# Performance work log

Hardware: AMD Instinct MI355X
Metric: run time of the kernel (lower is better)

Reference implementation:

```python
import jax, jax.numpy as jnp
import numpy as np

BS, S, N, C, H, CP, T, CT, NB = 1, 2, 2048, 128, 8, 16, 512, 384, 3
DH = C // H
INF = 1.0e8

def _ln(x, w, b, eps=1e-5):
    mu = jnp.mean(x, axis=-1, keepdims=True)
    var = jnp.var(x, axis=-1, keepdims=True)
    return (x - mu) * jax.lax.rsqrt(var + eps) * w + b

def _ln_na(x, eps=1e-5):
    mu = jnp.mean(x, axis=-1, keepdims=True)
    var = jnp.var(x, axis=-1, keepdims=True)
    return (x - mu) * jax.lax.rsqrt(var + eps)

def _betas(n):
    # query row l belongs to window centered at 32*(l//32)+16; keys within +/- n_keys//2=64
    l = jnp.arange(n)
    centers = (l // 32) * 32 + 16
    m = jnp.arange(n)
    ok = (m[None, :] >= (centers - 64)[:, None]) & (m[None, :] < (centers + 64)[:, None])
    return jnp.where(ok, 0.0, -INF).astype(jnp.float32)

def setup_inputs():
    key = jax.random.key(0)
    ks = iter(jax.random.split(key, 80))
    def W(*shape):
        return jax.random.normal(next(ks), shape, dtype=jnp.float32) * 0.05
    return {
        "atom_single": jax.random.normal(next(ks), (BS, S, N, C), dtype=jnp.float32),
        "atom_proj": jax.random.normal(next(ks), (BS, N, C), dtype=jnp.float32),
        "atom_pair": jax.random.normal(next(ks), (BS, N, N, CP), dtype=jnp.float32),
        "mask": jnp.ones((BS, N), jnp.float32),
        "tok_idx": jnp.sort(jax.random.randint(next(ks), (BS, N), 0, T), axis=-1),
        "aln_s_w": jnp.ones((NB, C), jnp.float32), "aln_s_b": jnp.zeros((NB, C), jnp.float32),
        "aln_gate_w": W(NB, C, C), "aln_gate_b": jnp.zeros((NB, C), jnp.float32),
        "aln_shift_w": W(NB, C, C),
        "q_w": W(NB, C, C), "q_b": jnp.zeros((NB, C), jnp.float32),
        "k_w": W(NB, C, C), "v_w": W(NB, C, C),
        "pair_ln_w": jnp.ones((NB, CP), jnp.float32), "pair_ln_b": jnp.zeros((NB, CP), jnp.float32),
        "pair_w": W(NB, CP, H),
        "gate_w": W(NB, C, C), "out_w": W(NB, C, C),
        "og_w": W(NB, C, C), "og_b": jnp.full((NB, C), -2.0, jnp.float32),
        "t_aln_s_w": jnp.ones((NB, C), jnp.float32), "t_aln_s_b": jnp.zeros((NB, C), jnp.float32),
        "t_aln_gate_w": W(NB, C, C), "t_aln_gate_b": jnp.zeros((NB, C), jnp.float32),
        "t_aln_shift_w": W(NB, C, C),
        "t_a_w": W(NB, C, 2 * C), "t_b_w": W(NB, C, 2 * C),
        "t_out_w": W(NB, 2 * C, C),
        "t_og_w": W(NB, C, C), "t_og_b": jnp.full((NB, C), -2.0, jnp.float32),
        "tok_w": W(C, CT),
    }

def _forward(atom_single, atom_proj, atom_pair, mask, tok_idx, aln_s_w, aln_s_b, aln_gate_w, aln_gate_b, aln_shift_w, q_w, q_b, k_w, v_w, pair_ln_w, pair_ln_b, pair_w, gate_w, out_w, og_w, og_b, t_aln_s_w, t_aln_s_b, t_aln_gate_w, t_aln_gate_b, t_aln_shift_w, t_a_w, t_b_w, t_out_w, t_og_w, t_og_b, tok_w):
    betas = _betas(N)[None, None, None]                        # [1,1,1,N,N]
    mask_bias = ((mask - 1.0) * INF)[:, None, None, None, :]   # [bs,1,1,1,N]
    s = atom_proj[:, None]                                     # [bs,1,N,C]
    a = atom_single                                            # [bs,S,N,C]
    for i in range(NB):
        # AttentionPairBias with AdaLN conditioning on s
        sn = _ln(s, aln_s_w[i], aln_s_b[i])
        a1 = jax.nn.sigmoid(sn @ aln_gate_w[i] + aln_gate_b[i]) * _ln_na(a) + sn @ aln_shift_w[i]
        q = (a1 @ q_w[i] + q_b[i]).reshape(BS, S, N, H, DH)
        k = (a1 @ k_w[i]).reshape(BS, S, N, H, DH)
        v = (a1 @ v_w[i]).reshape(BS, S, N, H, DH)
        zb = _ln(atom_pair, pair_ln_w[i], pair_ln_b[i]) @ pair_w[i]    # [bs,N,N,H]
        zb = jnp.transpose(zb, (0, 3, 1, 2))[:, None]                  # [bs,1,H,N,N]
        logits = jnp.einsum('bsqhd,bskhd->bshqk', q, k) / np.float32(np.sqrt(DH)) + zb + betas + mask_bias
        p = jax.nn.softmax(logits, axis=-1)
        o = jnp.einsum('bshqk,bskhd->bsqhd', p, v).reshape(BS, S, N, C)
        o = (jax.nn.sigmoid(a1 @ gate_w[i]) * o) @ out_w[i]
        a = a + jax.nn.sigmoid(sn @ og_w[i] + og_b[i]) * o
        # ConditionedTransitionBlock (SwiGLU with adaLN-Zero gating)
        sn2 = _ln(s, t_aln_s_w[i], t_aln_s_b[i])
        a2 = jax.nn.sigmoid(sn2 @ t_aln_gate_w[i] + t_aln_gate_b[i]) * _ln_na(a) + sn2 @ t_aln_shift_w[i]
        hidden = jax.nn.silu(a2 @ t_a_w[i]) * (a2 @ t_b_w[i])
        a = a + jax.nn.sigmoid(sn2 @ t_og_w[i] + t_og_b[i]) * (hidden @ t_out_w[i])
    # project to token dim, relu, scatter-mean atoms -> tokens
    q_tok = jax.nn.relu(a @ tok_w)                             # [bs,S,N,CT]
    oh = jax.nn.one_hot(tok_idx, T, dtype=q_tok.dtype)         # [bs,N,T]
    cnt = jnp.clip(jnp.sum(oh, axis=1), 1.0)                   # [bs,T]
    tok = jnp.einsum('bsnc,bnt->bstc', q_tok, oh) / cnt[:, None, :, None]
    return tok

def reference(atom_single, atom_proj, atom_pair, mask, tok_idx, aln_s_w, aln_s_b, aln_gate_w, aln_gate_b, aln_shift_w, q_w, q_b, k_w, v_w, pair_ln_w, pair_ln_b, pair_w, gate_w, out_w, og_w, og_b, t_aln_s_w, t_aln_s_b, t_aln_gate_w, t_aln_gate_b, t_aln_shift_w, t_a_w, t_b_w, t_out_w, t_og_w, t_og_b, tok_w):
    return _forward(atom_single, atom_proj, atom_pair, mask, tok_idx, aln_s_w, aln_s_b, aln_gate_w, aln_gate_b, aln_shift_w, q_w, q_b, k_w, v_w, pair_ln_w, pair_ln_b, pair_w, gate_w, out_w, og_w, og_b, t_aln_s_w, t_aln_s_b, t_aln_gate_w, t_aln_gate_b, t_aln_shift_w, t_a_w, t_b_w, t_out_w, t_og_w, t_og_b, tok_w)
```

## Files before the change

### kernel.cpp

```cpp
#include <hip/hip_runtime.h>
#include <math.h>

#define NATOM 2048
#define CD 128
#define SD 2
#define TT 512
#define CTD 384
#define NBI 3
#define MR 4096

typedef unsigned short ushortx;
typedef __attribute__((ext_vector_type(8))) short bf16x8;
typedef __attribute__((ext_vector_type(4))) float f32x4;
typedef __attribute__((ext_vector_type(4))) unsigned short us4;

__device__ __forceinline__ float sigm(float x){ return 1.0f/(1.0f+expf(-x)); }
__device__ __forceinline__ ushortx f2b(float f){
  union { float f; unsigned u; } v; v.f = f;
  unsigned r = v.u + 0x7fffu + ((v.u>>16)&1u);
  return (ushortx)(r>>16);
}
__device__ __forceinline__ float b2f(ushortx u){
  union { unsigned u; float f; } v; v.u = ((unsigned)u)<<16; return v.f;
}
union U8 { ushortx u[8]; float4 v; };

__device__ __forceinline__ void unpack8(float* dst, float4 v){
  U8 pk; pk.v = v;
  #pragma unroll
  for (int t=0;t<8;t++) dst[t] = b2f(pk.u[t]);
}

#define OFFB_W3T    0ll
#define OFFB_B3     589824ll
#define OFFB_WQKVGT 599040ll
#define OFFB_BQ     992256ll
#define OFFB_WOUTT  998400ll
#define OFFB_WABT   1096704ll
#define OFFB_WTOUTT 1489920ll
#define OFFB_WTOKT  1686528ll
#define OFFB_A1     1784832ll
#define OFFB_SNP    2833408ll
#define OFFB_A      12270592ll
#define OFFB_QKVG   14367744ll
#define OFFB_ZB     18562048ll
#define OFFB_QTOK   31144960ll

struct WPtrs {
  const float *aln_gate_w, *aln_gate_b, *aln_shift_w, *og_w, *og_b;
  const float *t_aln_gate_w, *t_aln_gate_b, *t_aln_shift_w, *t_og_w, *t_og_b;
  const float *q_w, *q_b, *k_w, *v_w, *gate_w, *out_w;
  const float *t_a_w, *t_b_w, *t_out_w, *tok_w;
};

__global__ __launch_bounds__(256) void prologue_kernel(WPtrs P, char* __restrict__ wsb,
  const float* __restrict__ atom_single, const float* __restrict__ atom_pair,
  const float* __restrict__ plw, const float* __restrict__ plb, const float* __restrict__ pw)
{
  int b = blockIdx.x;
  if (b < 3471){
    long long idx = (long long)b*256 + threadIdx.x;
    const long long s0=294912, s1=2304, s2=196608, s3=1536, s4=49152, s5=196608, s6=98304;
    if (idx < s0) {
      int which = (int)(idx/49152); int r = (int)(idx%49152); int n=r/128, k=r%128;
      int i = which>>1, t = which&1;
      const float* src;
      if (n<128)      src = (t?P.t_aln_gate_w :P.aln_gate_w ) + i*16384 + k*128 + n;
      else if (n<256) src = (t?P.t_aln_shift_w:P.aln_shift_w) + i*16384 + k*128 + (n-128);
      else            src = (t?P.t_og_w       :P.og_w       ) + i*16384 + k*128 + (n-256);
      ((ushortx*)(wsb+OFFB_W3T))[idx] = f2b(*src); return;
    }
    idx -= s0;
    if (idx < s1) {
      int which = (int)(idx/384); int col = (int)(idx%384); int i=which>>1, t=which&1;
      float v = 0.f;
      if (col<128)       v = (t?P.t_aln_gate_b:P.aln_gate_b)[i*128+col];
      else if (col>=256) v = (t?P.t_og_b      :P.og_b      )[i*128+col-256];
      ((float*)(wsb+OFFB_B3))[idx] = v; return;
    }
    idx -= s1;
    if (idx < s2) {
      int i = (int)(idx/65536); int r = (int)(idx%65536); int n=r/128, k=r%128;
      int seg = n>>7, c = n&127;
      const float* src = (seg==0?P.q_w: seg==1?P.k_w: seg==2?P.v_w: P.gate_w) + i*16384 + k*128 + c;
      ((ushortx*)(wsb+OFFB_WQKVGT))[idx] = f2b(*src); return;
    }
    idx -= s2;
    if (idx < s3) {
      int i = (int)(idx/512); int col = (int)(idx%512);
      ((float*)(wsb+OFFB_BQ))[idx] = (col<128) ? P.q_b[i*128+col] : 0.f; return;
    }
    idx -= s3;
    if (idx < s4) {
      int i = (int)(idx/16384); int r = (int)(idx%16384); int n=r/128, k=r%128;
      ((ushortx*)(wsb+OFFB_WOUTT))[idx] = f2b(P.out_w[i*16384 + k*128 + n]); return;
    }
    idx -= s4;
    if (idx < s5) {
      int i = (int)(idx/65536); int r = (int)(idx%65536); int n=r/128, k=r%128;
      const float* src = (n<256) ? P.t_a_w + i*32768 + k*256 + n
                                 : P.t_b_w + i*32768 + k*256 + (n-256);
      ((ushortx*)(wsb+OFFB_WABT))[idx] = f2b(*src); return;
    }
    idx -= s5;
    if (idx < s6) {
      int i = (int)(idx/32768); int r = (int)(idx%32768); int n=r/256, k=r%256;
      ((ushortx*)(wsb+OFFB_WTOUTT))[idx] = f2b(P.t_out_w[i*32768 + k*128 + n]); return;
    }
    idx -= s6;
    {
      int n = (int)(idx/128); int k = (int)(idx%128);
      ((ushortx*)(wsb+OFFB_WTOKT))[idx] = f2b(P.tok_w[k*384 + n]); return;
    }
  }
  if (b < 5519){
    int i = (b-3471)*256 + threadIdx.x;
    ((float*)(wsb+OFFB_A))[i] = atom_single[i];
    return;
  }
  {
    int idx = (b-5519)*256 + threadIdx.x;
    int q = idx>>7, j = idx&127;
    int m = (q & ~31) - 48 + j;
    bool ok = (m>=0 && m<NATOM);
    float x[16]; float mu=0.f, rs=0.f;
    if (ok){
      float s=0.f, sq=0.f;
      const float* p = atom_pair + ((long long)q*NATOM + m)*16;
      #pragma unroll
      for (int c=0;c<16;c++){ x[c]=p[c]; s+=x[c]; sq+=x[c]*x[c]; }
      mu = s*(1.f/16.f); float var = sq*(1.f/16.f)-mu*mu; rs = rsqrtf(var+1e-5f);
    }
    ushortx* zb = (ushortx*)(wsb+OFFB_ZB);
    #pragma unroll
    for (int it=0; it<NBI; it++){
      float out[8] = {0,0,0,0,0,0,0,0};
      if (ok){
        #pragma unroll
        for (int c=0;c<16;c++){
          float xn = (x[c]-mu)*rs*plw[it*16+c] + plb[it*16+c];
          #pragma unroll
          for (int h=0;h<8;h++) out[h] += xn * pw[it*128 + c*8 + h];
        }
      }
      #pragma unroll
      for (int h=0;h<8;h++)
        zb[(((long long)it*8+h)*NATOM + q)*128 + j] = f2b(out[h]);
    }
  }
}

__global__ __launch_bounds__(256) void attn_kernel(const ushortx* __restrict__ qkvg,
  const ushortx* __restrict__ zb, const float* __restrict__ mask, ushortx* __restrict__ og)
{
  int qb = blockIdx.x, h = blockIdx.y, s = blockIdx.z;
  int base = qb*32 - 48;
  __shared__ float Qs[32][20], Ks[128][20], Vs[128][20], Ls[32][132], maskb[128];
  __shared__ float redx[32][8], rowv[32];
  int tid = threadIdx.x;
  for (int idx=tid; idx<32*2; idx+=256){
    int r=idx>>1, d8=(idx&1)*8;
    float4 v = *(const float4*)&qkvg[((long long)(s*NATOM + qb*32 + r))*512 + h*16 + d8];
    unpack8(&Qs[r][d8], v);
  }
  for (int idx=tid; idx<512; idx+=256){
    int j = idx&127, d8 = ((idx>>7)&1)*8, kv = idx>>8;
    int m = base + j; int mc = m<0?0:(m>NATOM-1?NATOM-1:m);
    long long row = ((long long)(s*NATOM + mc))*512;
    float4 v = *(const float4*)&qkvg[row + (kv?256:128) + h*16 + d8];
    if (kv) unpack8(&Vs[j][d8], v); else unpack8(&Ks[j][d8], v);
  }
  if (tid < 128){
    int m = base + tid;
    maskb[tid] = (m>=0 && m<NATOM) ? (mask[m]-1.0f)*1e8f : -1e30f;
  }
  __syncthreads();
  int r = tid>>3, g = tid&7;
  {
    float4 q0=*(float4*)&Qs[r][0], q1=*(float4*)&Qs[r][4], q2=*(float4*)&Qs[r][8], q3=*(float4*)&Qs[r][12];
    const ushortx* zrow = zb + ((long long)h*NATOM + (qb*32+r))*128;
    #pragma unroll
    for (int j=g; j<128; j+=8){
      float4 k0=*(float4*)&Ks[j][0], k1=*(float4*)&Ks[j][4], k2=*(float4*)&Ks[j][8], k3=*(float4*)&Ks[j][12];
      float dot = q0.x*k0.x + q0.y*k0.y + q0.z*k0.z + q0.w*k0.w
                + q1.x*k1.x + q1.y*k1.y + q1.z*k1.z + q1.w*k1.w
                + q2.x*k2.x + q2.y*k2.y + q2.z*k2.z + q2.w*k2.w
                + q3.x*k3.x + q3.y*k3.y + q3.z*k3.z + q3.w*k3.w;
      Ls[r][j] = dot*0.25f + b2f(zrow[j]) + maskb[j];
    }
  }
  __syncthreads();
  float pmax = -1e30f;
  for (int j=g*16; j<g*16+16; j++) pmax = fmaxf(pmax, Ls[r][j]);
  redx[r][g] = pmax; __syncthreads();
  if (g==0){ float mx=redx[r][0]; for(int u=1;u<8;u++) mx=fmaxf(mx,redx[r][u]); rowv[r]=mx; }
  __syncthreads();
  float mx = rowv[r];
  float psum = 0.f;
  for (int j=g*16; j<g*16+16; j++){ float e = expf(Ls[r][j]-mx); Ls[r][j]=e; psum += e; }
  redx[r][g] = psum; __syncthreads();
  if (g==0){ float sm=0.f; for(int u=0;u<8;u++) sm+=redx[r][u]; rowv[r]=sm; }
  __syncthreads();
  {
    int q2=tid>>3, dg=(tid>>1)&3, jh=tid&1;
    float4 acc = make_float4(0.f,0.f,0.f,0.f);
    for (int j=jh*64; j<jh*64+64; j++){
      float p = Ls[q2][j];
      float4 v = *(float4*)&Vs[j][dg*4];
      acc.x += p*v.x; acc.y += p*v.y; acc.z += p*v.z; acc.w += p*v.w;
    }
    acc.x += __shfl_xor(acc.x,1); acc.y += __shfl_xor(acc.y,1);
    acc.z += __shfl_xor(acc.z,1); acc.w += __shfl_xor(acc.w,1);
    if (jh==0){
      long long mrow = (long long)(s*NATOM + qb*32 + q2);
      float inv = 1.0f / rowv[q2];
      us4 gt = *(const us4*)&qkvg[mrow*512 + 384 + h*16 + dg*4];
      us4 st;
      st[0] = f2b(sigm(b2f(gt[0]))*acc.x*inv);
      st[1] = f2b(sigm(b2f(gt[1]))*acc.y*inv);
      st[2] = f2b(sigm(b2f(gt[2]))*acc.z*inv);
      st[3] = f2b(sigm(b2f(gt[3]))*acc.w*inv);
      *(us4*)(og + mrow*128 + h*16 + dg*4) = st;
    }
  }
}

template<int AM, int BM>
__global__ __launch_bounds__(256) void gemm_f(
    const void* __restrict__ Asrc, long long strideA,
    const ushortx* __restrict__ B, long long strideB,
    const float* __restrict__ bias, long long strideBias,
    void* Cv, long long strideC,
    int M, int N, int K, int mode,
    const ushortx* __restrict__ gate, int gate_ld, int gate_coloff,
    const void* __restrict__ p1, const void* __restrict__ p2,
    const void* __restrict__ p3, const void* __restrict__ p4)
{
  constexpr int CG  = 256/BM;
  constexpr int XC  = 128/CG;
  constexpr int F4  = XC/8;
  constexpr int ACI = BM/32;
  int z = blockIdx.z;
  B += z*strideB;
  if (bias) bias += z*strideBias;
  float* C = (float*)Cv + z*strideC;
  ushortx* Cu = (ushortx*)Cv + z*strideC;
  __shared__ ushortx At[BM][136];
  __shared__ ushortx Bt[64][136];
  int tid = threadIdx.x;
  int rowBase = blockIdx.y*BM, colBase = blockIdx.x*64;
  int wave = tid>>6, lane = tid&63;
  int wr = (wave>>1)*(BM/2), wc = (wave&1)*32;
  int lr = lane&15, lk = (lane>>4)*8;
  f32x4 acc[ACI][2];
  #pragma unroll
  for (int i=0;i<ACI;i++)
    #pragma unroll
    for (int j=0;j<2;j++) acc[i][j] = (f32x4){0.f,0.f,0.f,0.f};

  int sr = tid/CG, q = tid%CG, cs = q*XC;
  int row = rowBase + sr;
  int bsr = tid>>2, bq = tid&3, bcs = bq*32;

  for (int kc=0; kc<K; kc+=128){
    if (kc) __syncthreads();
    if (AM==0){
      const ushortx* Ab = (const ushortx*)Asrc + z*strideA;
      const float4* ag = (const float4*)(Ab + (long long)row*K + kc + cs);
      #pragma unroll
      for (int u=0;u<F4;u++) *(float4*)&At[sr][cs+u*8] = ag[u];
    } else if (AM==3){
      const float* Af_ = (const float*)Asrc;
      const float4* ar = (const float4*)(Af_ + (long long)row*128 + cs);
      #pragma unroll
      for (int u=0;u<F4;u++){
        float4 a = ar[2*u], b = ar[2*u+1];
        U8 pk;
        pk.u[0]=f2b(a.x); pk.u[1]=f2b(a.y); pk.u[2]=f2b(a.z); pk.u[3]=f2b(a.w);
        pk.u[4]=f2b(b.x); pk.u[5]=f2b(b.y); pk.u[6]=f2b(b.z); pk.u[7]=f2b(b.w);
        *(float4*)&At[sr][cs+u*8] = pk.v;
      }
    } else if (AM==2){
      const ushortx* hp = (const ushortx*)Asrc;
      const float4* xr = (const float4*)(hp + (long long)row*512 + kc + cs);
      const float4* yr = (const float4*)(hp + (long long)row*512 + 256 + kc + cs);
      #pragma unroll
      for (int u=0;u<F4;u++){
        U8 xa, ya, pk;
        xa.v = xr[u]; ya.v = yr[u];
        #pragma unroll
        for (int t=0;t<8;t++){
          float x = b2f(xa.u[t]), y = b2f(ya.u[t]);
          pk.u[t] = f2b(x*sigm(x)*y);
        }
        *(float4*)&At[sr][cs+u*8] = pk.v;
      }
    } else {
      const float* arow = (const float*)Asrc + (long long)row*128;
      float x[XC]; float s=0.f, sq=0.f;
      const float4* ar = (const float4*)(arow + cs);
      #pragma unroll
      for (int u=0;u<XC/4;u++){
        float4 t = ar[u];
        x[4*u]=t.x; x[4*u+1]=t.y; x[4*u+2]=t.z; x[4*u+3]=t.w;
        s += t.x+t.y+t.z+t.w;
        sq += t.x*t.x+t.y*t.y+t.z*t.z+t.w*t.w;
      }
      #pragma unroll
      for (int off=1; off<CG; off<<=1){ s += __shfl_xor(s,off); sq += __shfl_xor(sq,off); }
      float mu = s*(1.f/128.f), var = sq*(1.f/128.f)-mu*mu;
      float rs = rsqrtf(var + 1e-5f);
      if (AM==1){
        const ushortx* sp = (const ushortx*)p1 + (long long)(row & (NATOM-1))*384;
        const float4* gr = (const float4*)(sp + cs);
        const float4* hr = (const float4*)(sp + 128 + cs);
        #pragma unroll
        for (int u=0;u<F4;u++){
          U8 ga, ha, pk;
          ga.v = gr[u]; ha.v = hr[u];
          #pragma unroll
          for (int t=0;t<8;t++)
            pk.u[t] = f2b(sigm(b2f(ga.u[t]))*((x[8*u+t]-mu)*rs) + b2f(ha.u[t]));
          *(float4*)&At[sr][cs+u*8] = pk.v;
        }
      } else {
        int iw = z>>1, tw = z&1;
        const float* w = (const float*)(tw?p3:p1) + iw*128;
        const float* b = (const float*)(tw?p4:p2) + iw*128;
        const float4* wrp = (const float4*)(w + cs);
        const float4* brp = (const float4*)(b + cs);
        #pragma unroll
        for (int u=0;u<F4;u++){
          float4 wa = wrp[2*u], wb = wrp[2*u+1];
          float4 ba = brp[2*u], bb = brp[2*u+1];
          U8 pk;
          pk.u[0]=f2b((x[8*u  ]-mu)*rs*wa.x+ba.x);
          pk.u[1]=f2b((x[8*u+1]-mu)*rs*wa.y+ba.y);
          pk.u[2]=f2b((x[8*u+2]-mu)*rs*wa.z+ba.z);
          pk.u[3]=f2b((x[8*u+3]-mu)*rs*wa.w+ba.w);
          pk.u[4]=f2b((x[8*u+4]-mu)*rs*wb.x+bb.x);
          pk.u[5]=f2b((x[8*u+5]-mu)*rs*wb.y+bb.y);
          pk.u[6]=f2b((x[8*u+6]-mu)*rs*wb.z+bb.z);
          pk.u[7]=f2b((x[8*u+7]-mu)*rs*wb.w+bb.w);
          *(float4*)&At[sr][cs+u*8] = pk.v;
        }
      }
    }
    {
      const float4* bg = (const float4*)(B + (long long)(colBase+bsr)*K + kc + bcs);
      #pragma unroll
      for (int u=0;u<4;u++) *(float4*)&Bt[bsr][bcs+u*8] = bg[u];
    }
    __syncthreads();
    #pragma unroll
    for (int ks=0; ks<4; ks++){
      bf16x8 b0 = *(const bf16x8*)&Bt[wc+lr][ks*32+lk];
      bf16x8 b1 = *(const bf16x8*)&Bt[wc+16+lr][ks*32+lk];
      #pragma unroll
      for (int i=0;i<ACI;i++){
        bf16x8 a = *(const bf16x8*)&At[wr+i*16+lr][ks*32+lk];
        acc[i][0] = __builtin_amdgcn_mfma_f32_16x16x32_bf16(a,b0,acc[i][0],0,0,0);
        acc[i][1] = __builtin_amdgcn_mfma_f32_16x16x32_bf16(a,b1,acc[i][1],0,0,0);
      }
    }
  }
  int crow0 = rowBase + wr + (lane>>4)*4;
  int ccol0 = colBase + wc + lr;
  #pragma unroll
  for (int i=0;i<ACI;i++){
    #pragma unroll
    for (int j=0;j<2;j++){
      int col = ccol0 + j*16;
      float bv = bias ? bias[col] : 0.f;
      #pragma unroll
      for (int rr=0; rr<4; rr++){
        int rrow = crow0 + i*16 + rr;
        float v = acc[i][j][rr] + bv;
        long long ci = (long long)rrow*N + col;
        if (mode==1) C[ci] = fmaxf(v, 0.f);
        else if (mode==2){
          int n = rrow & (NATOM-1);
          C[ci] += sigm(b2f(gate[(long long)n*gate_ld + gate_coloff + col])) * v;
        } else if (mode==3) Cu[ci] = f2b(v);
        else if (mode==4) Cu[ci] = f2b(fmaxf(v, 0.f));
        else C[ci] = v;
      }
    }
  }
}

__global__ __launch_bounds__(128) void tokagg_kernel(const int* __restrict__ tok_idx,
    const float* __restrict__ qtok, float* __restrict__ out)
{
  int t = blockIdx.x;
  int lo=0, hi=NATOM;
  while (lo<hi){ int mid=(lo+hi)>>1; if (tok_idx[mid] < t) lo=mid+1; else hi=mid; }
  int start = lo;
  lo = start; hi = NATOM;
  while (lo<hi){ int mid=(lo+hi)>>1; if (tok_idx[mid] <= t) lo=mid+1; else hi=mid; }
  int end = lo;
  int cnt = end - start;
  float inv = 1.0f / (float)(cnt>0 ? cnt : 1);
  for (int s=0; s<SD; s++)
    for (int c=threadIdx.x; c<CTD; c+=128){
      float acc = 0.f;
      for (int n=start; n<end; n++) acc += qtok[((long long)(s*NATOM+n))*CTD + c];
      out[(long long)(s*TT + t)*CTD + c] = acc*inv;
    }
}

extern "C" void kernel_launch(void* const* d_in, const int* in_sizes, int n_in,
                              void* d_out, int out_size, void* d_ws, size_t ws_size,
                              hipStream_t stream)
{
  const float* atom_single = (const float*)d_in[0];
  const float* atom_proj   = (const float*)d_in[1];
  const float* atom_pair   = (const float*)d_in[2];
  const float* mask        = (const float*)d_in[3];
  const int*   tok_idx     = (const int*)  d_in[4];
  const float* aln_s_w     = (const float*)d_in[5];
  const float* aln_s_b     = (const float*)d_in[6];
  const float* pair_ln_w   = (const float*)d_in[14];
  const float* pair_ln_b   = (const float*)d_in[15];
  const float* pair_w      = (const float*)d_in[16];
  const float* t_aln_s_w   = (const float*)d_in[21];
  const float* t_aln_s_b   = (const float*)d_in[22];

  char* wsb = (char*)d_ws;
  ushortx* W3T    = (ushortx*)(wsb+OFFB_W3T);
  float*   B3     = (float*)  (wsb+OFFB_B3);
  ushortx* WQKVGT = (ushortx*)(wsb+OFFB_WQKVGT);
  float*   BQ     = (float*)  (wsb+OFFB_BQ);
  ushortx* WOUTT  = (ushortx*)(wsb+OFFB_WOUTT);
  ushortx* WABT   = (ushortx*)(wsb+OFFB_WABT);
  ushortx* WTOUTT = (ushortx*)(wsb+OFFB_WTOUTT);
  ushortx* WTOKT  = (ushortx*)(wsb+OFFB_WTOKT);
  ushortx* A1     = (ushortx*)(wsb+OFFB_A1);
  ushortx* SNP    = (ushortx*)(wsb+OFFB_SNP);
  float*   Af     = (float*)  (wsb+OFFB_A);
  ushortx* QKVG   = (ushortx*)(wsb+OFFB_QKVG);
  ushortx* ZB     = (ushortx*)(wsb+OFFB_ZB);
  float*   QTOK   = (float*)  (wsb+OFFB_QTOK);

  WPtrs P;
  P.aln_gate_w=(const float*)d_in[7];  P.aln_gate_b=(const float*)d_in[8];  P.aln_shift_w=(const float*)d_in[9];
  P.og_w=(const float*)d_in[19]; P.og_b=(const float*)d_in[20];
  P.t_aln_gate_w=(const float*)d_in[23]; P.t_aln_gate_b=(const float*)d_in[24]; P.t_aln_shift_w=(const float*)d_in[25];
  P.t_og_w=(const float*)d_in[29]; P.t_og_b=(const float*)d_in[30];
  P.q_w=(const float*)d_in[10]; P.q_b=(const float*)d_in[11]; P.k_w=(const float*)d_in[12];
  P.v_w=(const float*)d_in[13]; P.gate_w=(const float*)d_in[17]; P.out_w=(const float*)d_in[18];
  P.t_a_w=(const float*)d_in[26]; P.t_b_w=(const float*)d_in[27]; P.t_out_w=(const float*)d_in[28];
  P.tok_w=(const float*)d_in[31];

  prologue_kernel<<<6543,256,0,stream>>>(P, wsb, atom_single, atom_pair,
      pair_ln_w, pair_ln_b, pair_w);
  gemm_f<4,64><<<dim3(6,32,6),256,0,stream>>>(atom_proj, 0, W3T, 49152ll,
      B3, 384ll, SNP, 786432ll, NATOM, 384, 128, 3, nullptr, 0, 0,
      aln_s_w, aln_s_b, t_aln_s_w, t_aln_s_b);

  for (int i=0;i<NBI;i++){
    const ushortx* snpA = SNP + (long long)(2*i)*786432;
    const ushortx* snpT = SNP + (long long)(2*i+1)*786432;
    gemm_f<1,64><<<dim3(8,64,1),256,0,stream>>>(Af, 0, WQKVGT + (long long)i*65536, 0,
        BQ + (long long)i*512, 0, QKVG, 0, MR, 512, 128, 3, nullptr, 0, 0,
        snpA, nullptr, nullptr, nullptr);
    attn_kernel<<<dim3(64,8,2),256,0,stream>>>(QKVG, ZB + (long long)i*2097152, mask, A1);
    gemm_f<0,32><<<dim3(2,128,1),256,0,stream>>>(A1, 0, WOUTT + (long long)i*16384, 0,
        nullptr, 0, Af, 0, MR, 128, 128, 2, snpA, 384, 256,
        nullptr, nullptr, nullptr, nullptr);
    gemm_f<1,64><<<dim3(8,64,1),256,0,stream>>>(Af, 0, WABT + (long long)i*65536, 0,
        nullptr, 0, QKVG, 0, MR, 512, 128, 3, nullptr, 0, 0,
        snpT, nullptr, nullptr, nullptr);
    gemm_f<2,32><<<dim3(2,128,1),256,0,stream>>>(QKVG, 0, WTOUTT + (long long)i*32768, 0,
        nullptr, 0, Af, 0, MR, 128, 256, 2, snpT, 384, 256,
        nullptr, nullptr, nullptr, nullptr);
  }
  gemm_f<3,64><<<dim3(6,64,1),256,0,stream>>>(Af, 0, WTOKT, 0, nullptr, 0,
      QTOK, 0, MR, CTD, 128, 1, nullptr, 0, 0,
      nullptr, nullptr, nullptr, nullptr);
  tokagg_kernel<<<TT,128,0,stream>>>(tok_idx, QTOK, (float*)d_out);
}
```

Baseline: 601.0 us.

## Fuse post-attention GEMM chain and next QKVG projection into one kernel

```diff
diff --git a/kernel.cpp b/kernel.cpp
--- a/kernel.cpp
+++ b/kernel.cpp
@@ -155,8 +155,11 @@
 {
   int qb = blockIdx.x, h = blockIdx.y, s = blockIdx.z;
   int base = qb*32 - 48;
-  __shared__ float Qs[32][20], Ks[128][20], Vs[128][20], Ls[32][132], maskb[128];
-  __shared__ float redx[32][8], rowv[32];
+  __shared__ __align__(16) float Qs[32][20];
+  __shared__ __align__(16) ushortx KsU[128][24];
+  __shared__ __align__(16) ushortx VsU[128][24];
+  __shared__ __align__(16) float Ls[32][132];
+  __shared__ float maskb[128], redx[32][8], rowv[32];
   int tid = threadIdx.x;
   for (int idx=tid; idx<32*2; idx+=256){
     int r=idx>>1, d8=(idx&1)*8;
@@ -168,7 +171,7 @@
     int m = base + j; int mc = m<0?0:(m>NATOM-1?NATOM-1:m);
     long long row = ((long long)(s*NATOM + mc))*512;
     float4 v = *(const float4*)&qkvg[row + (kv?256:128) + h*16 + d8];
-    if (kv) unpack8(&Vs[j][d8], v); else unpack8(&Ks[j][d8], v);
+    if (kv) *(float4*)&VsU[j][d8] = v; else *(float4*)&KsU[j][d8] = v;
   }
   if (tid < 128){
     int m = base + tid;
@@ -181,11 +184,11 @@
     const ushortx* zrow = zb + ((long long)h*NATOM + (qb*32+r))*128;
     #pragma unroll
     for (int j=g; j<128; j+=8){
-      float4 k0=*(float4*)&Ks[j][0], k1=*(float4*)&Ks[j][4], k2=*(float4*)&Ks[j][8], k3=*(float4*)&Ks[j][12];
-      float dot = q0.x*k0.x + q0.y*k0.y + q0.z*k0.z + q0.w*k0.w
-                + q1.x*k1.x + q1.y*k1.y + q1.z*k1.z + q1.w*k1.w
-                + q2.x*k2.x + q2.y*k2.y + q2.z*k2.z + q2.w*k2.w
-                + q3.x*k3.x + q3.y*k3.y + q3.z*k3.z + q3.w*k3.w;
+      U8 ka, kb; ka.v = *(const float4*)&KsU[j][0]; kb.v = *(const float4*)&KsU[j][8];
+      float dot = q0.x*b2f(ka.u[0]) + q0.y*b2f(ka.u[1]) + q0.z*b2f(ka.u[2]) + q0.w*b2f(ka.u[3])
+                + q1.x*b2f(ka.u[4]) + q1.y*b2f(ka.u[5]) + q1.z*b2f(ka.u[6]) + q1.w*b2f(ka.u[7])
+                + q2.x*b2f(kb.u[0]) + q2.y*b2f(kb.u[1]) + q2.z*b2f(kb.u[2]) + q2.w*b2f(kb.u[3])
+                + q3.x*b2f(kb.u[4]) + q3.y*b2f(kb.u[5]) + q3.z*b2f(kb.u[6]) + q3.w*b2f(kb.u[7]);
       Ls[r][j] = dot*0.25f + b2f(zrow[j]) + maskb[j];
     }
   }
@@ -206,8 +209,9 @@
     float4 acc = make_float4(0.f,0.f,0.f,0.f);
     for (int j=jh*64; j<jh*64+64; j++){
       float p = Ls[q2][j];
-      float4 v = *(float4*)&Vs[j][dg*4];
-      acc.x += p*v.x; acc.y += p*v.y; acc.z += p*v.z; acc.w += p*v.w;
+      us4 vv = *(const us4*)&VsU[j][dg*4];
+      acc.x += p*b2f(vv[0]); acc.y += p*b2f(vv[1]);
+      acc.z += p*b2f(vv[2]); acc.w += p*b2f(vv[3]);
     }
     acc.x += __shfl_xor(acc.x,1); acc.y += __shfl_xor(acc.y,1);
     acc.z += __shfl_xor(acc.z,1); acc.w += __shfl_xor(acc.w,1);
@@ -221,6 +225,152 @@
       st[2] = f2b(sigm(b2f(gt[2]))*acc.z*inv);
       st[3] = f2b(sigm(b2f(gt[3]))*acc.w*inv);
       *(us4*)(og + mrow*128 + h*16 + dg*4) = st;
+    }
+  }
+}
+
+template<int LAST>
+__global__ __launch_bounds__(256) void postattn_kernel(
+  float* __restrict__ Af, const ushortx* __restrict__ A1,
+  const ushortx* __restrict__ Wout,
+  const ushortx* __restrict__ Wab,
+  const ushortx* __restrict__ Wtout,
+  const ushortx* __restrict__ WN,
+  const float*   __restrict__ biasN,
+  const ushortx* __restrict__ snpA,
+  const ushortx* __restrict__ snpT,
+  const ushortx* __restrict__ snpN,
+  ushortx* __restrict__ QKVG,
+  float*   __restrict__ QTOK)
+{
+  __shared__ __align__(16) ushortx Bt[2][64][136];
+  __shared__ __align__(16) float   Afr[16][132];
+  __shared__ __align__(16) ushortx A2t[16][136];
+  __shared__ __align__(16) ushortx Ht[16][264];
+  __shared__ __align__(16) ushortx XX[16*264];
+  ushortx (*A1t)[136] = (ushortx(*)[136])XX;
+  ushortx (*Hs)[264]  = (ushortx(*)[264])XX;
+
+  int tid=threadIdx.x, rowBase=blockIdx.x*16;
+  int wave=tid>>6, lane=tid&63, lr=lane&15, lk=(lane>>4)*8;
+  int wc = wave*16;
+  int r=tid>>4, c8=(tid&15)*8;
+  long long grow = rowBase + r;
+  int sr=tid>>2, csB=(tid&3)*32;
+  int crow = (lane>>4)*4;
+
+  *(float4*)&A1t[r][c8] = *(const float4*)&A1[grow*128 + c8];
+  { const float4* ap=(const float4*)&Af[grow*128+c8];
+    *(float4*)&Afr[r][c8]=ap[0]; *(float4*)&Afr[r][c8+4]=ap[1]; }
+  const int NP = LAST ? 20 : 22;
+  {
+    const float4* bg = (const float4*)(Wout + (long long)sr*128 + csB);
+    #pragma unroll
+    for (int u=0;u<4;u++) *(float4*)&Bt[0][sr][csB+u*8] = bg[u];
+  }
+  f32x4 acc = (f32x4){0.f,0.f,0.f,0.f};
+  for (int p=0; p<NP; p++){
+    __syncthreads();
+    if (p+1 < NP){
+      int pn = p+1;
+      const ushortx* bsrc; long long bstride;
+      if (pn<2)      { bsrc = Wout  + (long long)(pn*64)*128;                      bstride=128; }
+      else if (pn<10){ bsrc = Wab   + (long long)((pn-2)*64)*128;                  bstride=128; }
+      else if (pn<14){ int q=pn-10; bsrc = Wtout + (long long)((q>>1)*64)*256 + (q&1)*128; bstride=256; }
+      else           { int q=pn-14; bsrc = WN    + (long long)(q*64)*128;          bstride=128; }
+      const float4* bg=(const float4*)(bsrc + (long long)sr*bstride + csB);
+      #pragma unroll
+      for (int u=0;u<4;u++) *(float4*)&Bt[pn&1][sr][csB+u*8] = bg[u];
+    }
+    if (p==2){
+      float x[8], s=0.f, sq=0.f;
+      #pragma unroll
+      for (int u=0;u<8;u++){ x[u]=Afr[r][c8+u]; s+=x[u]; sq+=x[u]*x[u]; }
+      #pragma unroll
+      for (int off=1; off<16; off<<=1){ s+=__shfl_xor(s,off); sq+=__shfl_xor(sq,off); }
+      float mu=s*(1.f/128.f), rs=rsqrtf(sq*(1.f/128.f)-mu*mu+1e-5f);
+      const ushortx* sp = snpT + (long long)(grow&2047)*384;
+      U8 ga,ha,pk; ga.v=*(const float4*)&sp[c8]; ha.v=*(const float4*)&sp[128+c8];
+      #pragma unroll
+      for (int t=0;t<8;t++) pk.u[t]=f2b(sigm(b2f(ga.u[t]))*((x[t]-mu)*rs)+b2f(ha.u[t]));
+      *(float4*)&A2t[r][c8]=pk.v;
+      __syncthreads();
+    }
+    if (p==14){
+      float x[8], s=0.f, sq=0.f;
+      #pragma unroll
+      for (int u=0;u<8;u++){ x[u]=Afr[r][c8+u]; s+=x[u]; sq+=x[u]*x[u]; }
+      { float4* ap=(float4*)&Af[grow*128+c8];
+        ap[0]=*(float4*)&Afr[r][c8]; ap[1]=*(float4*)&Afr[r][c8+4]; }
+      if (LAST){
+        U8 pk;
+        #pragma unroll
+        for (int t=0;t<8;t++) pk.u[t]=f2b(x[t]);
+        *(float4*)&A2t[r][c8]=pk.v;
+      } else {
+        #pragma unroll
+        for (int off=1; off<16; off<<=1){ s+=__shfl_xor(s,off); sq+=__shfl_xor(sq,off); }
+        float mu=s*(1.f/128.f), rs=rsqrtf(sq*(1.f/128.f)-mu*mu+1e-5f);
+        const ushortx* sp = snpN + (long long)(grow&2047)*384;
+        U8 ga,ha,pk; ga.v=*(const float4*)&sp[c8]; ha.v=*(const float4*)&sp[128+c8];
+        #pragma unroll
+        for (int t=0;t<8;t++) pk.u[t]=f2b(sigm(b2f(ga.u[t]))*((x[t]-mu)*rs)+b2f(ha.u[t]));
+        *(float4*)&A2t[r][c8]=pk.v;
+      }
+      __syncthreads();
+    }
+    if (p!=11 && p!=13) acc=(f32x4){0.f,0.f,0.f,0.f};
+    #pragma unroll
+    for (int ks=0; ks<4; ks++){
+      bf16x8 a;
+      if (p<2)       a = *(const bf16x8*)&A1t[lr][ks*32+lk];
+      else if (p<10) a = *(const bf16x8*)&A2t[lr][ks*32+lk];
+      else if (p<14){ int kc=(p-10)&1; a = *(const bf16x8*)&Hs[lr][kc*128+ks*32+lk]; }
+      else           a = *(const bf16x8*)&A2t[lr][ks*32+lk];
+      bf16x8 b = *(const bf16x8*)&Bt[p&1][wc+lr][ks*32+lk];
+      acc = __builtin_amdgcn_mfma_f32_16x16x32_bf16(a,b,acc,0,0,0);
+    }
+    if (p<2){
+      int ccol = p*64 + wc + lr;
+      #pragma unroll
+      for (int rr=0;rr<4;rr++){
+        int rrow=crow+rr;
+        float g=b2f(snpA[(long long)((rowBase+rrow)&2047)*384 + 256 + ccol]);
+        Afr[rrow][ccol]+=sigm(g)*acc[rr];
+      }
+    } else if (p<10){
+      int cp=p-2; int ccol=cp*64+wc+lr;
+      if (cp<4){
+        #pragma unroll
+        for (int rr=0;rr<4;rr++) Ht[crow+rr][ccol]=f2b(acc[rr]);
+      } else {
+        int hc=ccol-256;
+        #pragma unroll
+        for (int rr=0;rr<4;rr++){
+          float ha=b2f(Ht[crow+rr][hc]);
+          Hs[crow+rr][hc]=f2b(ha*sigm(ha)*acc[rr]);
+        }
+      }
+    } else if (p==11 || p==13){
+      int cp=(p-10)>>1; int ccol=cp*64+wc+lr;
+      #pragma unroll
+      for (int rr=0;rr<4;rr++){
+        int rrow=crow+rr;
+        float g=b2f(snpT[(long long)((rowBase+rrow)&2047)*384 + 256 + ccol]);
+        Afr[rrow][ccol]+=sigm(g)*acc[rr];
+      }
+    } else if (p>=14){
+      int q=p-14; int ccol=q*64+wc+lr;
+      if (LAST){
+        #pragma unroll
+        for (int rr=0;rr<4;rr++)
+          QTOK[(long long)(rowBase+crow+rr)*384 + ccol]=fmaxf(acc[rr],0.f);
+      } else {
+        float bv=biasN[ccol];
+        #pragma unroll
+        for (int rr=0;rr<4;rr++)
+          QKVG[(long long)(rowBase+crow+rr)*512 + ccol]=f2b(acc[rr]+bv);
+      }
     }
   }
 }
@@ -245,8 +395,8 @@
   if (bias) bias += z*strideBias;
   float* C = (float*)Cv + z*strideC;
   ushortx* Cu = (ushortx*)Cv + z*strideC;
-  __shared__ ushortx At[BM][136];
-  __shared__ ushortx Bt[64][136];
+  __shared__ __align__(16) ushortx At[BM][136];
+  __shared__ __align__(16) ushortx Bt[64][136];
   int tid = threadIdx.x;
   int rowBase = blockIdx.y*BM, colBase = blockIdx.x*64;
   int wave = tid>>6, lane = tid&63;
@@ -278,21 +428,6 @@
         U8 pk;
         pk.u[0]=f2b(a.x); pk.u[1]=f2b(a.y); pk.u[2]=f2b(a.z); pk.u[3]=f2b(a.w);
         pk.u[4]=f2b(b.x); pk.u[5]=f2b(b.y); pk.u[6]=f2b(b.z); pk.u[7]=f2b(b.w);
-        *(float4*)&At[sr][cs+u*8] = pk.v;
-      }
-    } else if (AM==2){
-      const ushortx* hp = (const ushortx*)Asrc;
-      const float4* xr = (const float4*)(hp + (long long)row*512 + kc + cs);
-      const float4* yr = (const float4*)(hp + (long long)row*512 + 256 + kc + cs);
-      #pragma unroll
-      for (int u=0;u<F4;u++){
-        U8 xa, ya, pk;
-        xa.v = xr[u]; ya.v = yr[u];
-        #pragma unroll
-        for (int t=0;t<8;t++){
-          float x = b2f(xa.u[t]), y = b2f(ya.u[t]);
-          pk.u[t] = f2b(x*sigm(x)*y);
-        }
         *(float4*)&At[sr][cs+u*8] = pk.v;
       }
     } else {
@@ -457,26 +592,24 @@
   gemm_f<4,64><<<dim3(6,32,6),256,0,stream>>>(atom_proj, 0, W3T, 49152ll,
       B3, 384ll, SNP, 786432ll, NATOM, 384, 128, 3, nullptr, 0, 0,
       aln_s_w, aln_s_b, t_aln_s_w, t_aln_s_b);
+  gemm_f<1,64><<<dim3(8,64,1),256,0,stream>>>(Af, 0, WQKVGT, 0,
+      BQ, 0, QKVG, 0, MR, 512, 128, 3, nullptr, 0, 0,
+      SNP, nullptr, nullptr, nullptr);
 
   for (int i=0;i<NBI;i++){
     const ushortx* snpA = SNP + (long long)(2*i)*786432;
     const ushortx* snpT = SNP + (long long)(2*i+1)*786432;
-    gemm_f<1,64><<<dim3(8,64,1),256,0,stream>>>(Af, 0, WQKVGT + (long long)i*65536, 0,
-        BQ + (long long)i*512, 0, QKVG, 0, MR, 512, 128, 3, nullptr, 0, 0,
-        snpA, nullptr, nullptr, nullptr);
     attn_kernel<<<dim3(64,8,2),256,0,stream>>>(QKVG, ZB + (long long)i*2097152, mask, A1);
-    gemm_f<0,32><<<dim3(2,128,1),256,0,stream>>>(A1, 0, WOUTT + (long long)i*16384, 0,
-        nullptr, 0, Af, 0, MR, 128, 128, 2, snpA, 384, 256,
-        nullptr, nullptr, nullptr, nullptr);
-    gemm_f<1,64><<<dim3(8,64,1),256,0,stream>>>(Af, 0, WABT + (long long)i*65536, 0,
-        nullptr, 0, QKVG, 0, MR, 512, 128, 3, nullptr, 0, 0,
-        snpT, nullptr, nullptr, nullptr);
-    gemm_f<2,32><<<dim3(2,128,1),256,0,stream>>>(QKVG, 0, WTOUTT + (long long)i*32768, 0,
-        nullptr, 0, Af, 0, MR, 128, 256, 2, snpT, 384, 256,
-        nullptr, nullptr, nullptr, nullptr);
-  }
-  gemm_f<3,64><<<dim3(6,64,1),256,0,stream>>>(Af, 0, WTOKT, 0, nullptr, 0,
-      QTOK, 0, MR, CTD, 128, 1, nullptr, 0, 0,
-      nullptr, nullptr, nullptr, nullptr);
+    if (i < NBI-1){
+      postattn_kernel<0><<<256,256,0,stream>>>(Af, A1,
+          WOUTT + (long long)i*16384, WABT + (long long)i*65536, WTOUTT + (long long)i*32768,
+          WQKVGT + (long long)(i+1)*65536, BQ + (long long)(i+1)*512,
+          snpA, snpT, SNP + (long long)(2*(i+1))*786432, QKVG, nullptr);
+    } else {
+      postattn_kernel<1><<<256,256,0,stream>>>(Af, A1,
+          WOUTT + (long long)i*16384, WABT + (long long)i*65536, WTOUTT + (long long)i*32768,
+          WTOKT, nullptr, snpA, snpT, nullptr, nullptr, QTOK);
+    }
+  }
   tokagg_kernel<<<TT,128,0,stream>>>(tok_idx, QTOK, (float*)d_out);
 }
```

Result: faster. 533.8 us (-11.2%).
